# Kernel optimization log

Hardware: AMD Instinct MI355X
Metric: run time of the kernel (lower is better)

The kernel has to match this reference:

```python
import jax, jax.numpy as jnp
import numpy as np

N = 50000
IN_DIM = 128
HIDDEN = 64
OUT_DIM = 10
HEADS = 4
NUM_LAYERS = 3
NEG_SLOPE = 0.2


def _glorot(key, shape):
    fan_in, fan_out = shape[0], shape[-1]
    lim = jnp.sqrt(6.0 / (fan_in + fan_out))
    return jax.random.uniform(key, shape, jnp.float32, -lim, lim)


def setup_inputs() -> dict:
    key = jax.random.key(0)
    ks = jax.random.split(key, 2 + 4 * NUM_LAYERS + 2)
    inp = {}
    inp["x"] = jax.random.normal(ks[0], (N, IN_DIM), jnp.float32)
    inp["edge_index"] = jax.random.randint(ks[1], (2, 800000), 0, N, jnp.int64)
    ki = 2
    for i in range(NUM_LAYERS):
        d_in = IN_DIM if i == 0 else HIDDEN
        inp[f"W{i}"] = _glorot(ks[ki], (d_in, HEADS * HIDDEN)); ki += 1
        inp[f"asrc{i}"] = _glorot(ks[ki], (HEADS, HIDDEN)); ki += 1
        inp[f"adst{i}"] = _glorot(ks[ki], (HEADS, HIDDEN)); ki += 1
        inp[f"b{i}"] = jnp.zeros((HIDDEN,), jnp.float32); ki += 1
    inp["fcW"] = _glorot(ks[ki], (HIDDEN, OUT_DIM)); ki += 1
    inp["fcb"] = jnp.zeros((OUT_DIM,), jnp.float32)
    return inp


def _gat_layer(x, W, a_src, a_dst, bias, src, dst):
    # x: [N, d_in] -> h: [N, H, D]
    h = (x @ W).reshape(N, HEADS, HIDDEN)
    al_s = jnp.einsum("nhd,hd->nh", h, a_src)  # [N, H]
    al_d = jnp.einsum("nhd,hd->nh", h, a_dst)  # [N, H]
    e = jax.nn.leaky_relu(al_s[src] + al_d[dst], NEG_SLOPE)  # [E, H]
    # segment softmax over incoming edges of each destination node
    m = jax.ops.segment_max(e, dst, num_segments=N)  # [N, H]
    ex = jnp.exp(e - m[dst])
    denom = jax.ops.segment_sum(ex, dst, num_segments=N)  # [N, H]
    alpha = ex / denom[dst]  # [E, H]
    # weighted scatter-add aggregation: [E,H,D] -> [N,H,D]
    out = jax.ops.segment_sum(alpha[:, :, None] * h[src], dst, num_segments=N)
    return out.mean(axis=1) + bias  # concat=False -> head mean, [N, HIDDEN]


def reference(x, edge_index, W0, asrc0, adst0, b0, W1, asrc1, adst1, b1,
              W2, asrc2, adst2, b2, fcW, fcb):
    # PyG GATConv default: add self-loops
    loops = jnp.arange(N, dtype=edge_index.dtype)
    src = jnp.concatenate([edge_index[0], loops])
    dst = jnp.concatenate([edge_index[1], loops])
    params = [(W0, asrc0, adst0, b0), (W1, asrc1, adst1, b1), (W2, asrc2, adst2, b2)]
    h = x
    for (W, a_s, a_d, b) in params:
        h = _gat_layer(h, W, a_s, a_d, b, src, dst)
        h = jax.nn.elu(h)
        # dropout p=0.3 is a no-op in eval mode
    return h @ fcW + fcb  # [N, OUT_DIM]
```

## Files before the change

kernel.cpp:

```cpp
#include <hip/hip_runtime.h>
#include <hip/hip_fp16.h>
#include <math.h>

#define N_NODES 50000
#define IN_DIM  128
#define HIDDEN  64
#define OUT_DIM 10
#define HEADS   4
#define E_RAW   800000
#define E_TOT   (E_RAW + N_NODES)
#define NEG_SLOPE 0.2f

#define NB_SCAN 196
#define NB_GEMH 782
#define NB_NODE 12500
#define NB_FILL 416

#define PAD 64

typedef _Float16 half8 __attribute__((ext_vector_type(8)));
typedef float floatx4 __attribute__((ext_vector_type(4)));
typedef float floatx2 __attribute__((ext_vector_type(2)));

#define PK_FMA(acc, x, e) \
    asm("v_pk_fma_f32 %0, %1, %2, %0" : "+v"(acc) : "v"(x), "v"(e))

__global__ void prep_kernel(const int* __restrict__ ei, int* __restrict__ cnt,
                            int* __restrict__ flag,
                            const float* __restrict__ X, __half* __restrict__ Xh,
                            const float* __restrict__ W0, const float* __restrict__ W1,
                            const float* __restrict__ W2,
                            __half* __restrict__ Wtf0, __half* __restrict__ Wtf1,
                            __half* __restrict__ Wtf2,
                            const float* __restrict__ as0, const float* __restrict__ ad0,
                            const float* __restrict__ as1, const float* __restrict__ ad1,
                            const float* __restrict__ as2, const float* __restrict__ ad2,
                            float* __restrict__ Wa0, float* __restrict__ Wa1,
                            float* __restrict__ Wa2) {
    int bid = blockIdx.x, t = threadIdx.x;
    if (bid < 196) {
        int i = bid * 256 + t;
        if (i < N_NODES) {
            cnt[i] = 0;
            const float4* X4 = (const float4*)(X + (size_t)i * 128);
            __half2* xh2 = (__half2*)(Xh + (size_t)i * 128);
#pragma unroll 8
            for (int k4 = 0; k4 < 32; k4++) {
                float4 v = X4[k4];
                xh2[k4 * 2]     = __float22half2_rn(make_float2(v.x, v.y));
                xh2[k4 * 2 + 1] = __float22half2_rn(make_float2(v.z, v.w));
            }
        }
    } else if (bid == 196) {
        __shared__ int anyv;
        if (t == 0) anyv = 0;
        __syncthreads();
        int idx = 2 * (t * 3100 + 17) + 1;
        if (ei[idx] != 0) atomicOr(&anyv, 1);
        __syncthreads();
        if (t == 0) flag[0] = anyv;
    } else if (bid < 229) {
        int i = (bid - 197) * 256 + t;
        int KC, DIN, f;
        const float* W; __half* Wtf;
        if (i < 4096)      { f = i;        KC = 16; DIN = 128; W = W0; Wtf = Wtf0; }
        else if (i < 6144) { f = i - 4096; KC = 8;  DIN = 64;  W = W1; Wtf = Wtf1; }
        else if (i < 8192) { f = i - 6144; KC = 8;  DIN = 64;  W = W2; Wtf = Wtf2; }
        else return;
        int lane = f & 63, kc = (f >> 6) % KC, ct = f / (64 * KC);
        int m = lane & 15, quad = lane >> 4;
        int col = ct * 16 + m;
        __half tmp[8];
#pragma unroll
        for (int j = 0; j < 8; j++) {
            int k = kc * 32 + quad * 8 + j;
            int h = k / DIN, kk = k % DIN;
            tmp[j] = __float2half(0.25f * W[kk * 256 + h * 64 + col]);
        }
        *(uint4*)(Wtf + (size_t)f * 8) = *(uint4*)tmp;
    } else {
        int b = bid - 229;
        int l, k;
        if (b < 128)      { l = 0; k = b; }
        else if (b < 192) { l = 1; k = b - 128; }
        else              { l = 2; k = b - 192; }
        const float* W  = (l == 0) ? W0 : (l == 1) ? W1 : W2;
        const float* as = (l == 0) ? as0 : (l == 1) ? as1 : as2;
        const float* ad = (l == 0) ? ad0 : (l == 1) ? ad1 : ad2;
        float* Wa       = (l == 0) ? Wa0 : (l == 1) ? Wa1 : Wa2;
        int h = t >> 6, d = t & 63;
        float wv = W[k * 256 + h * 64 + d];
        float ss = wv * as[h * 64 + d];
        float dd = wv * ad[h * 64 + d];
#pragma unroll
        for (int o = 1; o < 64; o <<= 1) {
            ss += __shfl_xor(ss, o, 64);
            dd += __shfl_xor(dd, o, 64);
        }
        if (d == 0) {
            Wa[k * 8 + h]     = ss;
            Wa[k * 8 + 4 + h] = dd;
        }
    }
}


__device__ __forceinline__ void al128_body(
    int n, const float* __restrict__ X, const float* __restrict__ Wa,
    float* __restrict__ AL) {
    if (n >= N_NODES) return;
    const float4* X4 = (const float4*)(X + (size_t)n * 128);
    float s[8];
#pragma unroll
    for (int j = 0; j < 8; j++) s[j] = 0.f;
#pragma unroll 4
    for (int k4 = 0; k4 < 32; k4++) {
        float4 v = X4[k4];
#pragma unroll
        for (int j = 0; j < 8; j++)
            s[j] += v.x * Wa[(k4 * 4 + 0) * 8 + j] + v.y * Wa[(k4 * 4 + 1) * 8 + j]
                  + v.z * Wa[(k4 * 4 + 2) * 8 + j] + v.w * Wa[(k4 * 4 + 3) * 8 + j];
    }
    *(float4*)(AL + n * 8)     = make_float4(s[0], s[1], s[2], s[3]);
    *(float4*)(AL + n * 8 + 4) = make_float4(s[4], s[5], s[6], s[7]);
}

__global__ void __launch_bounds__(256) fill_al(
    const int* __restrict__ ei, int* __restrict__ cnt,
    int* __restrict__ esrc_pad, const int* __restrict__ flag,
    const float* __restrict__ X, const float* __restrict__ Wa0,
    float* __restrict__ AL) {
    if (blockIdx.x < NB_FILL) {
        int base = blockIdx.x * 2048 + threadIdx.x;
        int sh = flag[0] ? 0 : 1;
        int srcs[8], dsts[8], poss[8];
        bool valid[8];
#pragma unroll
        for (int j = 0; j < 8; j++) {
            int t = base + j * 256;
            valid[j] = (t < E_TOT);
            srcs[j] = 0; dsts[j] = 0;
            if (valid[j]) {
                if (t < E_RAW) { srcs[j] = ei[t << sh]; dsts[j] = ei[(E_RAW + t) << sh]; }
                else           { srcs[j] = t - E_RAW;   dsts[j] = srcs[j]; }
            }
        }
#pragma unroll
        for (int j = 0; j < 8; j++)
            if (valid[j]) poss[j] = atomicAdd(&cnt[dsts[j]], 1);
#pragma unroll
        for (int j = 0; j < 8; j++)
            if (valid[j] && poss[j] < PAD)
                esrc_pad[(dsts[j] << 6) + poss[j]] = srcs[j];
    } else {
        int n = (blockIdx.x - NB_FILL) * 256 + threadIdx.x;
        al128_body(n, X, Wa0, AL);
    }
}

__device__ __forceinline__ void agg_prologue(
    int n, int c, int wave, int lane,
    const float* __restrict__ AL, const int* __restrict__ esrc,
    floatx2 (*ldsE2)[64][4], int (*ldsS)[64], float* dn) {
    const float4* AL4 = (const float4*)AL;
    float4 ad = AL4[n * 2 + 1];
    int my_s = 0;
    float4 myE = make_float4(0.f, 0.f, 0.f, 0.f);
    if (lane < c) {
        my_s = esrc[(n << 6) + lane];
        float4 as = AL4[my_s * 2];
        float v0 = as.x + ad.x; v0 = fmaxf(v0, NEG_SLOPE * v0);
        float v1 = as.y + ad.y; v1 = fmaxf(v1, NEG_SLOPE * v1);
        float v2 = as.z + ad.z; v2 = fmaxf(v2, NEG_SLOPE * v2);
        float v3 = as.w + ad.w; v3 = fmaxf(v3, NEG_SLOPE * v3);
        myE = make_float4(__expf(v0), __expf(v1), __expf(v2), __expf(v3));
    }
    floatx2* row = ldsE2[wave][lane];
    row[0] = floatx2{myE.x, myE.x};
    row[1] = floatx2{myE.y, myE.y};
    row[2] = floatx2{myE.z, myE.z};
    row[3] = floatx2{myE.w, myE.w};
    ldsS[wave][lane] = my_s;
    float d0 = myE.x, d1 = myE.y, d2 = myE.z, d3 = myE.w;
#pragma unroll
    for (int o = 1; o < 64; o <<= 1) {
        d0 += __shfl_xor(d0, o, 64);
        d1 += __shfl_xor(d1, o, 64);
        d2 += __shfl_xor(d2, o, 64);
        d3 += __shfl_xor(d3, o, 64);
    }
    dn[0] = d0; dn[1] = d1; dn[2] = d2; dn[3] = d3;
}

__global__ void __launch_bounds__(256) agg_x128(
    const __half* __restrict__ X16, const float* __restrict__ AL,
    const int* __restrict__ cnt, const int* __restrict__ esrc,
    __half* __restrict__ AGG) {
    __shared__ floatx2 ldsE2[4][64][4];
    __shared__ int     ldsS[4][64];
    int wave = threadIdx.x >> 6, lane = threadIdx.x & 63;
    int n = blockIdx.x * 4 + wave;
    int c = cnt[n]; if (c > PAD) c = PAD;

    float dn[4];
    agg_prologue(n, c, wave, lane, AL, esrc, ldsE2, ldsS, dn);

    floatx2 aP[4] = {floatx2{0.f, 0.f}, floatx2{0.f, 0.f},
                     floatx2{0.f, 0.f}, floatx2{0.f, 0.f}};
    int lx = lane << 1;
    int nIter = (c + 7) >> 3;
    for (int it = 0; it < nIter; ++it) {
        int j0 = it << 3;
#pragma unroll
        for (int k = 0; k < 8; k++) {
            int e = j0 + k;
            int sv = ldsS[wave][e];
            float2 xv = __half22float2(*(const __half2*)(X16 + (sv << 7) + lx));
            floatx2 xp = floatx2{xv.x, xv.y};
            floatx2 e0 = ldsE2[wave][e][0];
            floatx2 e1 = ldsE2[wave][e][1];
            floatx2 e2 = ldsE2[wave][e][2];
            floatx2 e3 = ldsE2[wave][e][3];
            PK_FMA(aP[0], xp, e0);
            PK_FMA(aP[1], xp, e1);
            PK_FMA(aP[2], xp, e2);
            PK_FMA(aP[3], xp, e3);
        }
    }
#pragma unroll
    for (int h = 0; h < 4; h++) {
        float inv = 1.f / dn[h];
        *(__half2*)(AGG + n * 512 + h * 128 + lx) =
            __float22half2_rn(make_float2(aP[h].x * inv, aP[h].y * inv));
    }
}

__global__ void __launch_bounds__(256) agg_x64(
    const __half* __restrict__ X16, const float* __restrict__ AL,
    const int* __restrict__ cnt, const int* __restrict__ esrc,
    __half* __restrict__ AGG) {
    __shared__ floatx2 ldsE2[4][64][4];
    __shared__ int     ldsS[4][64];
    int wave = threadIdx.x >> 6, lane = threadIdx.x & 63;
    int n = blockIdx.x * 4 + wave;
    int c = cnt[n]; if (c > PAD) c = PAD;

    float dn[4];
    agg_prologue(n, c, wave, lane, AL, esrc, ldsE2, ldsS, dn);

    int hlf = lane >> 5;
    int dp = lane & 31;
    int dx = dp << 1;
    floatx2 aP[4] = {floatx2{0.f, 0.f}, floatx2{0.f, 0.f},
                     floatx2{0.f, 0.f}, floatx2{0.f, 0.f}};
    int nIter = (c + 15) >> 4;
    for (int it = 0; it < nIter; ++it) {
        int e0b = (it << 4) + hlf;
#pragma unroll
        for (int k = 0; k < 8; k++) {
            int e = e0b + (k << 1);
            int sv = ldsS[wave][e];
            float2 xv = __half22float2(*(const __half2*)(X16 + (sv << 6) + dx));
            floatx2 xp = floatx2{xv.x, xv.y};
            floatx2 e0 = ldsE2[wave][e][0];
            floatx2 e1 = ldsE2[wave][e][1];
            floatx2 e2 = ldsE2[wave][e][2];
            floatx2 e3 = ldsE2[wave][e][3];
            PK_FMA(aP[0], xp, e0);
            PK_FMA(aP[1], xp, e1);
            PK_FMA(aP[2], xp, e2);
            PK_FMA(aP[3], xp, e3);
        }
    }
#pragma unroll
    for (int h = 0; h < 4; h++) {
        aP[h].x += __shfl_xor(aP[h].x, 32, 64);
        aP[h].y += __shfl_xor(aP[h].y, 32, 64);
    }
    int h0 = hlf << 1;
#pragma unroll
    for (int hh = 0; hh < 2; hh++) {
        int h = h0 + hh;
        float inv = 1.f / dn[h];
        *(__half2*)(AGG + n * 256 + h * 64 + dx) =
            __float22half2_rn(make_float2(aP[h].x * inv, aP[h].y * inv));
    }
}

template <int K>
__global__ void __launch_bounds__(256) gemm_out(
    const __half* __restrict__ AGG, const __half* __restrict__ Wtf,
    const float* __restrict__ bias, const float* __restrict__ Wa,
    __half* __restrict__ X16, float* __restrict__ ALout,
    const float* __restrict__ fcW, const float* __restrict__ fcb,
    float* __restrict__ OUT) {
    __shared__ _Float16 lds[16384];
    const int KC = K / 32;
    const int NCHUNK = (K == 512) ? 2 : 1;
    const int CTC = 4 / NCHUNK;
    int t = threadIdx.x;
    int w = t >> 6, lane = t & 63;
    int m = lane & 15, quad = lane >> 4;
    int n0 = blockIdx.x * 64;
    int nr = n0 + w * 16 + m;
    int nc = (nr < N_NODES) ? nr : (N_NODES - 1);

    half8 afrag[KC];
#pragma unroll
    for (int kc = 0; kc < KC; kc++)
        afrag[kc] = *(const half8*)(AGG + (size_t)nc * K + kc * 32 + quad * 8);

    floatx4 accs[4];
    const uint4* Wg = (const uint4*)Wtf;
#pragma unroll
    for (int c = 0; c < NCHUNK; c++) {
        __syncthreads();
        uint4* dstl = (uint4*)lds;
        const uint4* srcg = Wg + (size_t)c * 2048;
#pragma unroll
        for (int q = 0; q < 8; q++) dstl[t + 256 * q] = srcg[t + 256 * q];
        __syncthreads();
#pragma unroll
        for (int ctl = 0; ctl < CTC; ctl++) {
            floatx4 acc = {0.f, 0.f, 0.f, 0.f};
#pragma unroll
            for (int kc = 0; kc < KC; kc++) {
                half8 b = *(const half8*)&lds[((ctl * KC + kc) * 64 + lane) * 8];
                acc = __builtin_amdgcn_mfma_f32_16x16x32_f16(afrag[kc], b, acc, 0, 0, 0);
            }
            accs[c * CTC + ctl] = acc;
        }
    }
    float vv[4][4];
#pragma unroll
    for (int ct = 0; ct < 4; ct++) {
        float bv = bias[ct * 16 + m];
#pragma unroll
        for (int i = 0; i < 4; i++) {
            float v = accs[ct][i] + bv;
            vv[ct][i] = v > 0.f ? v : (__expf(v) - 1.f);
        }
    }
    int nodeBase = n0 + w * 16 + quad * 4;
    if (X16) {
#pragma unroll
        for (int ct = 0; ct < 4; ct++) {
            int col = ct * 16 + m;
#pragma unroll
            for (int i = 0; i < 4; i++) {
                int node = nodeBase + i;
                if (node < N_NODES)
                    X16[(size_t)node * 64 + col] = __float2half(vv[ct][i]);
            }
        }
    }
    if (ALout) {
        float war[4][8];
#pragma unroll
        for (int ct = 0; ct < 4; ct++) {
            const float4* wp = (const float4*)(Wa + (ct * 16 + m) * 8);
            float4 a = wp[0], b = wp[1];
            war[ct][0] = a.x; war[ct][1] = a.y; war[ct][2] = a.z; war[ct][3] = a.w;
            war[ct][4] = b.x; war[ct][5] = b.y; war[ct][6] = b.z; war[ct][7] = b.w;
        }
#pragma unroll
        for (int i = 0; i < 4; i++) {
            int node = nodeBase + i;
            float alm = 0.f;
#pragma unroll
            for (int j = 0; j < 8; j++) {
                float s = vv[0][i] * war[0][j] + vv[1][i] * war[1][j]
                        + vv[2][i] * war[2][j] + vv[3][i] * war[3][j];
                s += __shfl_xor(s, 1, 64);
                s += __shfl_xor(s, 2, 64);
                s += __shfl_xor(s, 4, 64);
                s += __shfl_xor(s, 8, 64);
                if (j == (m & 7)) alm = s;
            }
            if (m < 8 && node < N_NODES) ALout[(size_t)node * 8 + m] = alm;
        }
    }
    if (OUT) {
        float* ldsF = (float*)lds;
        __syncthreads();
        int lr0 = w * 16 + quad * 4;
#pragma unroll
        for (int ct = 0; ct < 4; ct++) {
            int col = ct * 16 + m;
#pragma unroll
            for (int i = 0; i < 4; i++)
                ldsF[(lr0 + i) * 66 + col] = vv[ct][i];
        }
        __syncthreads();
        for (int idx = t; idx < 640; idx += 256) {
            int nl = idx / 10, c = idx % 10;
            int node = n0 + nl;
            if (node < N_NODES) {
                float s = fcb[c];
#pragma unroll 8
                for (int d = 0; d < 64; d++)
                    s += ldsF[nl * 66 + d] * fcW[d * 10 + c];
                OUT[(size_t)node * 10 + c] = s;
            }
        }
    }
}

extern "C" void kernel_launch(void* const* d_in, const int* in_sizes, int n_in,
                              void* d_out, int out_size, void* d_ws, size_t ws_size,
                              hipStream_t stream) {
    const float* x     = (const float*)d_in[0];
    const int*   ei    = (const int*)d_in[1];
    const float* W[3]    = {(const float*)d_in[2], (const float*)d_in[6], (const float*)d_in[10]};
    const float* asrc[3] = {(const float*)d_in[3], (const float*)d_in[7], (const float*)d_in[11]};
    const float* adst[3] = {(const float*)d_in[4], (const float*)d_in[8], (const float*)d_in[12]};
    const float* bias[3] = {(const float*)d_in[5], (const float*)d_in[9], (const float*)d_in[13]};
    const float* fcW = (const float*)d_in[14];
    const float* fcb = (const float*)d_in[15];
    float* out = (float*)d_out;

    char* ws = (char*)d_ws;
    size_t off = 0;
    auto alloc = [&](size_t bytes) {
        void* p = ws + off;
        off = (off + bytes + 255) & ~(size_t)255;
        return p;
    };
    __half* AGG     = (__half*)alloc((size_t)N_NODES * 512 * 2);
    float*  AL      = (float*)alloc((size_t)N_NODES * 8 * 4);
    __half* Xh0     = (__half*)alloc((size_t)N_NODES * 128 * 2);
    __half* X16     = (__half*)alloc((size_t)N_NODES * 64 * 2);
    __half* Wtf0    = (__half*)alloc(4096 * 8 * 2);
    __half* Wtf1    = (__half*)alloc(2048 * 8 * 2);
    __half* Wtf2    = (__half*)alloc(2048 * 8 * 2);
    float*  Wa0     = (float*)alloc(128 * 8 * 4);
    float*  Wa1     = (float*)alloc(64 * 8 * 4);
    float*  Wa2     = (float*)alloc(64 * 8 * 4);
    int* cnt      = (int*)alloc((size_t)N_NODES * 4);
    int* esrc_pad = (int*)alloc((size_t)N_NODES * PAD * 4);
    int* flag     = (int*)alloc(256 * 4);

    prep_kernel<<<485, 256, 0, stream>>>(ei, cnt, flag, x, Xh0,
                                         W[0], W[1], W[2],
                                         Wtf0, Wtf1, Wtf2,
                                         asrc[0], adst[0], asrc[1], adst[1],
                                         asrc[2], adst[2], Wa0, Wa1, Wa2);
    fill_al<<<NB_FILL + NB_SCAN, 256, 0, stream>>>(ei, cnt, esrc_pad, flag,
                                                   x, Wa0, AL);
    agg_x128<<<NB_NODE, 256, 0, stream>>>(Xh0, AL, cnt, esrc_pad, AGG);
    gemm_out<512><<<NB_GEMH, 256, 0, stream>>>(AGG, Wtf0, bias[0], Wa1,
                                               X16, AL, nullptr, nullptr, nullptr);
    agg_x64<<<NB_NODE, 256, 0, stream>>>(X16, AL, cnt, esrc_pad, AGG);
    gemm_out<256><<<NB_GEMH, 256, 0, stream>>>(AGG, Wtf1, bias[1], Wa2,
                                               X16, AL, nullptr, nullptr, nullptr);
    agg_x64<<<NB_NODE, 256, 0, stream>>>(X16, AL, cnt, esrc_pad, AGG);
    gemm_out<256><<<NB_GEMH, 256, 0, stream>>>(AGG, Wtf2, bias[2], nullptr,
                                               nullptr, nullptr, fcW, fcb, out);
}
```

Measured before the change: 330.8 us.

## Split edges across half-waves in agg_x128 and move fp16 conversions into fill_al

The first-layer aggregation kernel now has the two half-waves of each wavefront work on alternating edges. Each lane loads four fp16 features (8 bytes) per gather instead of two, and the partial sums are combined with a cross-half shuffle before writing. This is meant to widen the gather loads and halve the serial edge-loop length, at the cost of extra shuffles and a split output write. Separately, the X-to-fp16 conversion and the weight-fragment preparation move from prep_kernel into fill_al. That shortens the serial prep kernel and lets this work overlap with the edge-fill atomics.

```diff
diff --git a/kernel.cpp b/kernel.cpp
--- a/kernel.cpp
+++ b/kernel.cpp
@@ -27,11 +27,8 @@
 
 __global__ void prep_kernel(const int* __restrict__ ei, int* __restrict__ cnt,
                             int* __restrict__ flag,
-                            const float* __restrict__ X, __half* __restrict__ Xh,
                             const float* __restrict__ W0, const float* __restrict__ W1,
                             const float* __restrict__ W2,
-                            __half* __restrict__ Wtf0, __half* __restrict__ Wtf1,
-                            __half* __restrict__ Wtf2,
                             const float* __restrict__ as0, const float* __restrict__ ad0,
                             const float* __restrict__ as1, const float* __restrict__ ad1,
                             const float* __restrict__ as2, const float* __restrict__ ad2,
@@ -40,17 +37,7 @@
     int bid = blockIdx.x, t = threadIdx.x;
     if (bid < 196) {
         int i = bid * 256 + t;
-        if (i < N_NODES) {
-            cnt[i] = 0;
-            const float4* X4 = (const float4*)(X + (size_t)i * 128);
-            __half2* xh2 = (__half2*)(Xh + (size_t)i * 128);
-#pragma unroll 8
-            for (int k4 = 0; k4 < 32; k4++) {
-                float4 v = X4[k4];
-                xh2[k4 * 2]     = __float22half2_rn(make_float2(v.x, v.y));
-                xh2[k4 * 2 + 1] = __float22half2_rn(make_float2(v.z, v.w));
-            }
-        }
+        if (i < N_NODES) cnt[i] = 0;
     } else if (bid == 196) {
         __shared__ int anyv;
         if (t == 0) anyv = 0;
@@ -59,27 +46,8 @@
         if (ei[idx] != 0) atomicOr(&anyv, 1);
         __syncthreads();
         if (t == 0) flag[0] = anyv;
-    } else if (bid < 229) {
-        int i = (bid - 197) * 256 + t;
-        int KC, DIN, f;
-        const float* W; __half* Wtf;
-        if (i < 4096)      { f = i;        KC = 16; DIN = 128; W = W0; Wtf = Wtf0; }
-        else if (i < 6144) { f = i - 4096; KC = 8;  DIN = 64;  W = W1; Wtf = Wtf1; }
-        else if (i < 8192) { f = i - 6144; KC = 8;  DIN = 64;  W = W2; Wtf = Wtf2; }
-        else return;
-        int lane = f & 63, kc = (f >> 6) % KC, ct = f / (64 * KC);
-        int m = lane & 15, quad = lane >> 4;
-        int col = ct * 16 + m;
-        __half tmp[8];
-#pragma unroll
-        for (int j = 0; j < 8; j++) {
-            int k = kc * 32 + quad * 8 + j;
-            int h = k / DIN, kk = k % DIN;
-            tmp[j] = __float2half(0.25f * W[kk * 256 + h * 64 + col]);
-        }
-        *(uint4*)(Wtf + (size_t)f * 8) = *(uint4*)tmp;
     } else {
-        int b = bid - 229;
+        int b = bid - 197;
         int l, k;
         if (b < 128)      { l = 0; k = b; }
         else if (b < 192) { l = 1; k = b - 128; }
@@ -128,8 +96,12 @@
 __global__ void __launch_bounds__(256) fill_al(
     const int* __restrict__ ei, int* __restrict__ cnt,
     int* __restrict__ esrc_pad, const int* __restrict__ flag,
-    const float* __restrict__ X, const float* __restrict__ Wa0,
-    float* __restrict__ AL) {
+    const float* __restrict__ X, __half* __restrict__ Xh,
+    const float* __restrict__ W0, const float* __restrict__ W1,
+    const float* __restrict__ W2,
+    __half* __restrict__ Wtf0, __half* __restrict__ Wtf1,
+    __half* __restrict__ Wtf2,
+    const float* __restrict__ Wa0, float* __restrict__ AL) {
     if (blockIdx.x < NB_FILL) {
         int base = blockIdx.x * 2048 + threadIdx.x;
         int sh = flag[0] ? 0 : 1;
@@ -152,8 +124,39 @@
         for (int j = 0; j < 8; j++)
             if (valid[j] && poss[j] < PAD)
                 esrc_pad[(dsts[j] << 6) + poss[j]] = srcs[j];
+    } else if (blockIdx.x < NB_FILL + 196) {
+        int i = (blockIdx.x - NB_FILL) * 256 + threadIdx.x;
+        if (i < N_NODES) {
+            const float4* X4 = (const float4*)(X + (size_t)i * 128);
+            __half2* xh2 = (__half2*)(Xh + (size_t)i * 128);
+#pragma unroll 8
+            for (int k4 = 0; k4 < 32; k4++) {
+                float4 v = X4[k4];
+                xh2[k4 * 2]     = __float22half2_rn(make_float2(v.x, v.y));
+                xh2[k4 * 2 + 1] = __float22half2_rn(make_float2(v.z, v.w));
+            }
+        }
+    } else if (blockIdx.x < NB_FILL + 228) {
+        int i = (blockIdx.x - NB_FILL - 196) * 256 + threadIdx.x;
+        int KC, DIN, f;
+        const float* W; __half* Wtf;
+        if (i < 4096)      { f = i;        KC = 16; DIN = 128; W = W0; Wtf = Wtf0; }
+        else if (i < 6144) { f = i - 4096; KC = 8;  DIN = 64;  W = W1; Wtf = Wtf1; }
+        else if (i < 8192) { f = i - 6144; KC = 8;  DIN = 64;  W = W2; Wtf = Wtf2; }
+        else return;
+        int lane = f & 63, kc = (f >> 6) % KC, ct = f / (64 * KC);
+        int m = lane & 15, quad = lane >> 4;
+        int col = ct * 16 + m;
+        __half tmp[8];
+#pragma unroll
+        for (int j = 0; j < 8; j++) {
+            int k = kc * 32 + quad * 8 + j;
+            int h = k / DIN, kk = k % DIN;
+            tmp[j] = __float2half(0.25f * W[kk * 256 + h * 64 + col]);
+        }
+        *(uint4*)(Wtf + (size_t)f * 8) = *(uint4*)tmp;
     } else {
-        int n = (blockIdx.x - NB_FILL) * 256 + threadIdx.x;
+        int n = (blockIdx.x - NB_FILL - 228) * 256 + threadIdx.x;
         al128_body(n, X, Wa0, AL);
     }
 }
@@ -205,33 +208,53 @@
     float dn[4];
     agg_prologue(n, c, wave, lane, AL, esrc, ldsE2, ldsS, dn);
 
-    floatx2 aP[4] = {floatx2{0.f, 0.f}, floatx2{0.f, 0.f},
-                     floatx2{0.f, 0.f}, floatx2{0.f, 0.f}};
-    int lx = lane << 1;
-    int nIter = (c + 7) >> 3;
+    int hlf = lane >> 5;
+    int dp  = lane & 31;
+    int dx  = dp << 2;
+    floatx2 a01[4] = {floatx2{0.f,0.f}, floatx2{0.f,0.f},
+                      floatx2{0.f,0.f}, floatx2{0.f,0.f}};
+    floatx2 a23[4] = {floatx2{0.f,0.f}, floatx2{0.f,0.f},
+                      floatx2{0.f,0.f}, floatx2{0.f,0.f}};
+    int nIter = (c + 15) >> 4;
     for (int it = 0; it < nIter; ++it) {
-        int j0 = it << 3;
+        int e0b = (it << 4) + hlf;
 #pragma unroll
         for (int k = 0; k < 8; k++) {
-            int e = j0 + k;
+            int e = e0b + (k << 1);
             int sv = ldsS[wave][e];
-            float2 xv = __half22float2(*(const __half2*)(X16 + (sv << 7) + lx));
-            floatx2 xp = floatx2{xv.x, xv.y};
+            uint2 raw = *(const uint2*)(X16 + (sv << 7) + dx);
+            float2 x01 = __half22float2(*(__half2*)&raw.x);
+            float2 x23 = __half22float2(*(__half2*)&raw.y);
+            floatx2 xp01 = floatx2{x01.x, x01.y};
+            floatx2 xp23 = floatx2{x23.x, x23.y};
             floatx2 e0 = ldsE2[wave][e][0];
             floatx2 e1 = ldsE2[wave][e][1];
             floatx2 e2 = ldsE2[wave][e][2];
             floatx2 e3 = ldsE2[wave][e][3];
-            PK_FMA(aP[0], xp, e0);
-            PK_FMA(aP[1], xp, e1);
-            PK_FMA(aP[2], xp, e2);
-            PK_FMA(aP[3], xp, e3);
+            PK_FMA(a01[0], xp01, e0); PK_FMA(a23[0], xp23, e0);
+            PK_FMA(a01[1], xp01, e1); PK_FMA(a23[1], xp23, e1);
+            PK_FMA(a01[2], xp01, e2); PK_FMA(a23[2], xp23, e2);
+            PK_FMA(a01[3], xp01, e3); PK_FMA(a23[3], xp23, e3);
         }
     }
 #pragma unroll
     for (int h = 0; h < 4; h++) {
+        a01[h].x += __shfl_xor(a01[h].x, 32, 64);
+        a01[h].y += __shfl_xor(a01[h].y, 32, 64);
+        a23[h].x += __shfl_xor(a23[h].x, 32, 64);
+        a23[h].y += __shfl_xor(a23[h].y, 32, 64);
+    }
+    int h0 = hlf << 1;
+#pragma unroll
+    for (int hh = 0; hh < 2; hh++) {
+        int h = h0 + hh;
         float inv = 1.f / dn[h];
-        *(__half2*)(AGG + n * 512 + h * 128 + lx) =
-            __float22half2_rn(make_float2(aP[h].x * inv, aP[h].y * inv));
+        __half2 o01 = __float22half2_rn(make_float2(a01[h].x * inv, a01[h].y * inv));
+        __half2 o23 = __float22half2_rn(make_float2(a23[h].x * inv, a23[h].y * inv));
+        uint2 ov;
+        ov.x = *(unsigned int*)&o01;
+        ov.y = *(unsigned int*)&o23;
+        *(uint2*)(AGG + n * 512 + h * 128 + dx) = ov;
     }
 }
 
@@ -440,13 +463,13 @@
     int* esrc_pad = (int*)alloc((size_t)N_NODES * PAD * 4);
     int* flag     = (int*)alloc(256 * 4);
 
-    prep_kernel<<<485, 256, 0, stream>>>(ei, cnt, flag, x, Xh0,
+    prep_kernel<<<453, 256, 0, stream>>>(ei, cnt, flag,
                                          W[0], W[1], W[2],
-                                         Wtf0, Wtf1, Wtf2,
                                          asrc[0], adst[0], asrc[1], adst[1],
                                          asrc[2], adst[2], Wa0, Wa1, Wa2);
-    fill_al<<<NB_FILL + NB_SCAN, 256, 0, stream>>>(ei, cnt, esrc_pad, flag,
-                                                   x, Wa0, AL);
+    fill_al<<<NB_FILL + 196 + 32 + 196, 256, 0, stream>>>(
+        ei, cnt, esrc_pad, flag, x, Xh0,
+        W[0], W[1], W[2], Wtf0, Wtf1, Wtf2, Wa0, AL);
     agg_x128<<<NB_NODE, 256, 0, stream>>>(Xh0, AL, cnt, esrc_pad, AGG);
     gemm_out<512><<<NB_GEMH, 256, 0, stream>>>(AGG, Wtf0, bias[0], Wa1,
                                                X16, AL, nullptr, nullptr, nullptr);
```

Result: slower. 349.6 us (+5.7%).
